# Kernel optimization log

Measured on AMD Instinct MI355X. Metric: run time of the kernel, lower is better.

Reference implementation:

```python
import jax, jax.numpy as jnp
import numpy as np

NUM_CLASSES = 8
IGNORE_INDEX = 255
GAMMA = 2.0
CE_W = 1.0
D_W = 0.1
MIN_CLASS_PIXELS = 10
EPS = 1e-05


def setup_inputs() -> dict:
    key = jax.random.key(0)
    k1, k2 = jax.random.split(key)
    outputs = jax.random.normal(k1, (16, NUM_CLASSES, 512, 512), dtype=jnp.float32)
    targets = jax.random.randint(k2, (16, 512, 512), 0, NUM_CLASSES, dtype=jnp.int64)
    return {"outputs": outputs, "targets": targets}


def reference(outputs, targets):
    B, C, H, W = outputs.shape
    probs = jax.nn.softmax(outputs, axis=1)            # [B,C,H,W]
    logp = jax.nn.log_softmax(outputs, axis=1)         # [B,C,H,W]
    focal = (1.0 - probs) ** GAMMA * logp              # [B,C,H,W]

    valid = targets != IGNORE_INDEX                    # [B,H,W]
    tgt_safe = jnp.where(valid, targets, 0)

    # Focal-weighted NLL: -focal[b, target, h, w], mean over non-ignored pixels
    picked = jnp.take_along_axis(focal, tgt_safe[:, None], axis=1)[:, 0]  # [B,H,W]
    vf = valid.astype(focal.dtype)
    ce_loss = -(picked * vf).sum() / vf.sum()

    # Soft dice, per image, classes 1..C-1, only classes with >MIN_CLASS_PIXELS pixels
    N = H * W
    probs_f = probs.reshape(B, C, N)                   # [B,C,N]
    tgt_f = tgt_safe.reshape(B, N)
    valid_f = valid.reshape(B, N)
    cls_ids = jnp.arange(C)
    t_onehot = ((tgt_f[:, None, :] == cls_ids[None, :, None]) & valid_f[:, None, :]).astype(probs.dtype)  # [B,C,N]
    p_masked = probs_f * valid_f[:, None, :].astype(probs.dtype)

    inter = (p_masked * t_onehot).sum(axis=2)          # [B,C]
    psum = p_masked.sum(axis=2)                        # [B,C]
    tsum = t_onehot.sum(axis=2)                        # [B,C]

    per_cls = 1.0 - (2.0 * inter + EPS) / (psum + tsum + EPS)   # [B,C]
    per_cls = jnp.where(tsum > MIN_CLASS_PIXELS, per_cls, 0.0)
    d_loss = (per_cls[:, 1:].sum(axis=1) / (C - 1)).mean()

    return CE_W * ce_loss + D_W * d_loss
```

## Files before the change

### kernel.cpp

```cpp
#include <hip/hip_runtime.h>

#define BB 16
#define CC 8
#define HW (512 * 512)
#define IGNORE_IDX 255
#define EPS_F 1e-5f
#define MINPIX 10.0f

#define BPI 64
#define NTHR 256
#define NBLK (BB * BPI)
#define PPB (HW / BPI)

#define OFF_INTER 0
#define OFF_PSUM  8192
#define OFF_TSUM  16384
#define OFF_CE    24576
#define OFF_CNT   (24576 + NBLK)

__device__ __forceinline__ float wave_red(float v) {
#pragma unroll
    for (int o = 32; o > 0; o >>= 1) v += __shfl_xor(v, o, 64);
    return v;
}

__global__ __launch_bounds__(NTHR) void focal_stage1(
    const float* __restrict__ logits, const int* __restrict__ tgt,
    float* __restrict__ ws)
{
    const int b     = blockIdx.x / BPI;
    const int chunk = blockIdx.x % BPI;
    const float* base = logits + (size_t)b * (CC * HW);
    const int*   tb   = tgt    + (size_t)b * HW;
    const int start = chunk * PPB;

    float psum[8]  = {0.f,0.f,0.f,0.f,0.f,0.f,0.f,0.f};
    float inter[8] = {0.f,0.f,0.f,0.f,0.f,0.f,0.f,0.f};
    int   tcnt[8]  = {0,0,0,0,0,0,0,0};
    float ce = 0.f;
    int   cnt = 0;

    for (int it = 0; it < PPB; it += NTHR * 4) {
        const int pix = start + it + (int)threadIdx.x * 4;
        const int4 t4 = *reinterpret_cast<const int4*>(tb + pix);
        float4 v[8];
#pragma unroll
        for (int c = 0; c < 8; ++c)
            v[c] = *reinterpret_cast<const float4*>(base + (size_t)c * HW + pix);

#pragma unroll
        for (int j = 0; j < 4; ++j) {
            const int t = (&t4.x)[j];
            float x[8];
#pragma unroll
            for (int c = 0; c < 8; ++c) x[c] = (&v[c].x)[j];

            float m = x[0];
#pragma unroll
            for (int c = 1; c < 8; ++c) m = fmaxf(m, x[c]);

            float e[8];
            float s = 0.f;
#pragma unroll
            for (int c = 0; c < 8; ++c) { e[c] = __expf(x[c] - m); s += e[c]; }
            const float inv = 1.0f / s;

            const bool valid = (t != IGNORE_IDX);
            float xt = 0.f, et = 0.f;
#pragma unroll
            for (int c = 0; c < 8; ++c) {
                const float pc = e[c] * inv;
                psum[c] += valid ? pc : 0.f;
                const bool hit = valid && (t == c);
                inter[c] += hit ? pc : 0.f;
                tcnt[c]  += hit ? 1 : 0;
                xt = (t == c) ? x[c] : xt;
                et = (t == c) ? e[c] : et;
            }
            const float pt    = et * inv;
            const float logpt = (xt - m) - __logf(s);
            const float omp   = 1.f - pt;
            ce  += valid ? -(omp * omp) * logpt : 0.f;
            cnt += valid ? 1 : 0;
        }
    }

    __shared__ float sm[4][26];
    const int wave = threadIdx.x >> 6;
    const int lane = threadIdx.x & 63;

    float red[26];
#pragma unroll
    for (int c = 0; c < 8; ++c) red[c]      = inter[c];
#pragma unroll
    for (int c = 0; c < 8; ++c) red[8 + c]  = psum[c];
#pragma unroll
    for (int c = 0; c < 8; ++c) red[16 + c] = (float)tcnt[c];
    red[24] = ce;
    red[25] = (float)cnt;

#pragma unroll
    for (int k = 0; k < 26; ++k) {
        const float r = wave_red(red[k]);
        if (lane == 0) sm[wave][k] = r;
    }
    __syncthreads();

    const int tid = threadIdx.x;
    if (tid < 26) {
        const float tot = sm[0][tid] + sm[1][tid] + sm[2][tid] + sm[3][tid];
        if (tid < 8)
            ws[OFF_INTER + ((b * CC + tid) * BPI) + chunk] = tot;
        else if (tid < 16)
            ws[OFF_PSUM + ((b * CC + (tid - 8)) * BPI) + chunk] = tot;
        else if (tid < 24)
            ws[OFF_TSUM + ((b * CC + (tid - 16)) * BPI) + chunk] = tot;
        else if (tid == 24)
            ws[OFF_CE + blockIdx.x] = tot;
        else
            ws[OFF_CNT + blockIdx.x] = tot;
    }
}

__global__ __launch_bounds__(NTHR) void focal_stage2(
    const float* __restrict__ ws, float* __restrict__ out)
{
    const int tid = threadIdx.x;

    float dval = 0.f;
    if (tid < BB * CC) {
        const int c = tid & 7;
        const int off = tid * BPI;
        float I = 0.f, P = 0.f, T = 0.f;
        for (int k = 0; k < BPI; ++k) {
            I += ws[OFF_INTER + off + k];
            P += ws[OFF_PSUM  + off + k];
            T += ws[OFF_TSUM  + off + k];
        }
        if (c >= 1 && T > MINPIX)
            dval = 1.f - (2.f * I + EPS_F) / (P + T + EPS_F);
    }

    float ce = 0.f, cn = 0.f;
    for (int k = tid; k < NBLK; k += NTHR) {
        ce += ws[OFF_CE + k];
        cn += ws[OFF_CNT + k];
    }

    dval = wave_red(dval);
    ce   = wave_red(ce);
    cn   = wave_red(cn);

    __shared__ float sd[3][4];
    const int wave = tid >> 6;
    const int lane = tid & 63;
    if (lane == 0) { sd[0][wave] = dval; sd[1][wave] = ce; sd[2][wave] = cn; }
    __syncthreads();

    if (tid == 0) {
        const float D  = sd[0][0] + sd[0][1] + sd[0][2] + sd[0][3];
        const float CE = sd[1][0] + sd[1][1] + sd[1][2] + sd[1][3];
        const float CN = sd[2][0] + sd[2][1] + sd[2][2] + sd[2][3];
        out[0] = (CE / CN) + 0.1f * (D / ((CC - 1) * (float)BB));
    }
}

extern "C" void kernel_launch(void* const* d_in, const int* in_sizes, int n_in,
                              void* d_out, int out_size, void* d_ws, size_t ws_size,
                              hipStream_t stream)
{
    const float* logits = (const float*)d_in[0];
    const int*   tgt    = (const int*)d_in[1];
    float*       ws     = (float*)d_ws;
    float*       out    = (float*)d_out;

    focal_stage1<<<NBLK, NTHR, 0, stream>>>(logits, tgt, ws);
    focal_stage2<<<1, NTHR, 0, stream>>>(ws, out);
}
```

Baseline: 42.83 us.

## Split stage1 into one-iteration blocks and parallelize stage2 reduction across 1024 threads

Result: slower. 66.88 us (+56.1%).

```diff
diff --git a/kernel.cpp b/kernel.cpp
--- a/kernel.cpp
+++ b/kernel.cpp
@@ -7,16 +7,16 @@
 #define EPS_F 1e-5f
 #define MINPIX 10.0f
 
-#define BPI 64
+#define BPI 256
 #define NTHR 256
 #define NBLK (BB * BPI)
 #define PPB (HW / BPI)
 
 #define OFF_INTER 0
-#define OFF_PSUM  8192
-#define OFF_TSUM  16384
-#define OFF_CE    24576
-#define OFF_CNT   (24576 + NBLK)
+#define OFF_PSUM  32768
+#define OFF_TSUM  65536
+#define OFF_CE    98304
+#define OFF_CNT   (98304 + NBLK)
 
 __device__ __forceinline__ float wave_red(float v) {
 #pragma unroll
@@ -32,7 +32,13 @@
     const int chunk = blockIdx.x % BPI;
     const float* base = logits + (size_t)b * (CC * HW);
     const int*   tb   = tgt    + (size_t)b * HW;
-    const int start = chunk * PPB;
+    const int pix = chunk * PPB + (int)threadIdx.x * 4;
+
+    const int4 t4 = *reinterpret_cast<const int4*>(tb + pix);
+    float4 v[8];
+#pragma unroll
+    for (int c = 0; c < 8; ++c)
+        v[c] = *reinterpret_cast<const float4*>(base + (size_t)c * HW + pix);
 
     float psum[8]  = {0.f,0.f,0.f,0.f,0.f,0.f,0.f,0.f};
     float inter[8] = {0.f,0.f,0.f,0.f,0.f,0.f,0.f,0.f};
@@ -40,49 +46,40 @@
     float ce = 0.f;
     int   cnt = 0;
 
-    for (int it = 0; it < PPB; it += NTHR * 4) {
-        const int pix = start + it + (int)threadIdx.x * 4;
-        const int4 t4 = *reinterpret_cast<const int4*>(tb + pix);
-        float4 v[8];
 #pragma unroll
-        for (int c = 0; c < 8; ++c)
-            v[c] = *reinterpret_cast<const float4*>(base + (size_t)c * HW + pix);
+    for (int j = 0; j < 4; ++j) {
+        const int t = (&t4.x)[j];
+        float x[8];
+#pragma unroll
+        for (int c = 0; c < 8; ++c) x[c] = (&v[c].x)[j];
 
+        float m = x[0];
 #pragma unroll
-        for (int j = 0; j < 4; ++j) {
-            const int t = (&t4.x)[j];
-            float x[8];
+        for (int c = 1; c < 8; ++c) m = fmaxf(m, x[c]);
+
+        float e[8];
+        float s = 0.f;
 #pragma unroll
-            for (int c = 0; c < 8; ++c) x[c] = (&v[c].x)[j];
+        for (int c = 0; c < 8; ++c) { e[c] = __expf(x[c] - m); s += e[c]; }
+        const float inv = 1.0f / s;
 
-            float m = x[0];
+        const bool valid = (t != IGNORE_IDX);
+        float xt = 0.f, et = 0.f;
 #pragma unroll
-            for (int c = 1; c < 8; ++c) m = fmaxf(m, x[c]);
-
-            float e[8];
-            float s = 0.f;
-#pragma unroll
-            for (int c = 0; c < 8; ++c) { e[c] = __expf(x[c] - m); s += e[c]; }
-            const float inv = 1.0f / s;
-
-            const bool valid = (t != IGNORE_IDX);
-            float xt = 0.f, et = 0.f;
-#pragma unroll
-            for (int c = 0; c < 8; ++c) {
-                const float pc = e[c] * inv;
-                psum[c] += valid ? pc : 0.f;
-                const bool hit = valid && (t == c);
-                inter[c] += hit ? pc : 0.f;
-                tcnt[c]  += hit ? 1 : 0;
-                xt = (t == c) ? x[c] : xt;
-                et = (t == c) ? e[c] : et;
-            }
-            const float pt    = et * inv;
-            const float logpt = (xt - m) - __logf(s);
-            const float omp   = 1.f - pt;
-            ce  += valid ? -(omp * omp) * logpt : 0.f;
-            cnt += valid ? 1 : 0;
+        for (int c = 0; c < 8; ++c) {
+            const float pc = e[c] * inv;
+            psum[c] += valid ? pc : 0.f;
+            const bool hit = valid && (t == c);
+            inter[c] += hit ? pc : 0.f;
+            tcnt[c]  += hit ? 1 : 0;
+            xt = (t == c) ? x[c] : xt;
+            et = (t == c) ? e[c] : et;
         }
+        const float pt    = et * inv;
+        const float logpt = (xt - m) - __logf(s);
+        const float omp   = 1.f - pt;
+        ce  += valid ? -(omp * omp) * logpt : 0.f;
+        cnt += valid ? 1 : 0;
     }
 
     __shared__ float sm[4][26];
@@ -122,45 +119,62 @@
     }
 }
 
-__global__ __launch_bounds__(NTHR) void focal_stage2(
+#define NTHR2 1024
+
+__global__ __launch_bounds__(NTHR2) void focal_stage2(
     const float* __restrict__ ws, float* __restrict__ out)
 {
-    const int tid = threadIdx.x;
+    const int tid  = threadIdx.x;
+    const int wave = tid >> 6;
+    const int lane = tid & 63;
+
+    const int pair = tid >> 3;
+    const int sub  = tid & 7;
+    float I = 0.f, P = 0.f, T = 0.f;
+    {
+        const int off = pair * BPI + sub * (BPI / 8);
+#pragma unroll
+        for (int k = 0; k < BPI / 8; k += 4) {
+            const float4 i4 = *reinterpret_cast<const float4*>(&ws[OFF_INTER + off + k]);
+            const float4 p4 = *reinterpret_cast<const float4*>(&ws[OFF_PSUM  + off + k]);
+            const float4 t4 = *reinterpret_cast<const float4*>(&ws[OFF_TSUM  + off + k]);
+            I += i4.x + i4.y + i4.z + i4.w;
+            P += p4.x + p4.y + p4.z + p4.w;
+            T += t4.x + t4.y + t4.z + t4.w;
+        }
+    }
+#pragma unroll
+    for (int o = 1; o < 8; o <<= 1) {
+        I += __shfl_xor(I, o, 64);
+        P += __shfl_xor(P, o, 64);
+        T += __shfl_xor(T, o, 64);
+    }
 
     float dval = 0.f;
-    if (tid < BB * CC) {
-        const int c = tid & 7;
-        const int off = tid * BPI;
-        float I = 0.f, P = 0.f, T = 0.f;
-        for (int k = 0; k < BPI; ++k) {
-            I += ws[OFF_INTER + off + k];
-            P += ws[OFF_PSUM  + off + k];
-            T += ws[OFF_TSUM  + off + k];
-        }
-        if (c >= 1 && T > MINPIX)
-            dval = 1.f - (2.f * I + EPS_F) / (P + T + EPS_F);
-    }
+    const int c = pair & 7;
+    if (sub == 0 && c >= 1 && T > MINPIX)
+        dval = 1.f - (2.f * I + EPS_F) / (P + T + EPS_F);
 
-    float ce = 0.f, cn = 0.f;
-    for (int k = tid; k < NBLK; k += NTHR) {
-        ce += ws[OFF_CE + k];
-        cn += ws[OFF_CNT + k];
+    float ce, cn;
+    {
+        const float4 c4 = *reinterpret_cast<const float4*>(&ws[OFF_CE  + tid * 4]);
+        const float4 n4 = *reinterpret_cast<const float4*>(&ws[OFF_CNT + tid * 4]);
+        ce = c4.x + c4.y + c4.z + c4.w;
+        cn = n4.x + n4.y + n4.z + n4.w;
     }
 
     dval = wave_red(dval);
     ce   = wave_red(ce);
     cn   = wave_red(cn);
 
-    __shared__ float sd[3][4];
-    const int wave = tid >> 6;
-    const int lane = tid & 63;
+    __shared__ float sd[3][16];
     if (lane == 0) { sd[0][wave] = dval; sd[1][wave] = ce; sd[2][wave] = cn; }
     __syncthreads();
 
     if (tid == 0) {
-        const float D  = sd[0][0] + sd[0][1] + sd[0][2] + sd[0][3];
-        const float CE = sd[1][0] + sd[1][1] + sd[1][2] + sd[1][3];
-        const float CN = sd[2][0] + sd[2][1] + sd[2][2] + sd[2][3];
+        float D = 0.f, CE = 0.f, CN = 0.f;
+#pragma unroll
+        for (int w = 0; w < 16; ++w) { D += sd[0][w]; CE += sd[1][w]; CN += sd[2][w]; }
         out[0] = (CE / CN) + 0.1f * (D / ((CC - 1) * (float)BB));
     }
 }
@@ -175,5 +189,5 @@
     float*       out    = (float*)d_out;
 
     focal_stage1<<<NBLK, NTHR, 0, stream>>>(logits, tgt, ws);
-    focal_stage2<<<1, NTHR, 0, stream>>>(ws, out);
+    focal_stage2<<<1, NTHR2, 0, stream>>>(ws, out);
 }
```
